# Optimization experiments

Measured on AMD Instinct MI355X. Metric: run time of the kernel, lower is better.

## Reference

```python
import jax, jax.numpy as jnp
import numpy as np

N, E, B = 100000, 1600000, 4
NODE_DIM, EDGE_DIM, H, L, C_DIM = 3, 1, 128, 6, 100


def _mlp2(x, w1, b1, w2, b2):
    # Linear -> ReLU -> Linear
    return jax.nn.relu(x @ w1 + b1) @ w2 + b2


def setup_inputs() -> dict:
    key = jax.random.key(0)
    ks = jax.random.split(key, 32)
    s = 0.02
    inp = {
        "x": jax.random.normal(ks[0], (N, NODE_DIM), jnp.float32),
        "edge_index": jax.random.randint(ks[1], (2, E), 0, N, jnp.int64),
        "edge_attr": jax.random.uniform(ks[2], (E, EDGE_DIM), jnp.float32),
        "t": jax.random.uniform(ks[3], (B,), jnp.float32),
        "batch": jnp.sort(jax.random.randint(ks[4], (N,), 0, B, jnp.int64)),
        "condition": jax.random.normal(ks[5], (B, C_DIM), jnp.float32),
        # input_mlp
        "in_w1": jax.random.normal(ks[6], (NODE_DIM, H), jnp.float32) * s,
        "in_b1": jnp.zeros((H,), jnp.float32),
        "in_w2": jax.random.normal(ks[7], (H, H), jnp.float32) * s,
        "in_b2": jnp.zeros((H,), jnp.float32),
        # time_mlp
        "t_w1": jax.random.normal(ks[8], (1, H), jnp.float32) * s,
        "t_b1": jnp.zeros((H,), jnp.float32),
        "t_w2": jax.random.normal(ks[9], (H, H), jnp.float32) * s,
        "t_b2": jnp.zeros((H,), jnp.float32),
        # condition_mlp
        "c_w1": jax.random.normal(ks[10], (C_DIM, H), jnp.float32) * s,
        "c_b1": jnp.zeros((H,), jnp.float32),
        "c_w2": jax.random.normal(ks[11], (H, H), jnp.float32) * s,
        "c_b2": jnp.zeros((H,), jnp.float32),
        # 6 EdgeConv layers, stacked
        "convW1": jax.random.normal(ks[12], (L, 2 * H + EDGE_DIM, H), jnp.float32) * s,
        "convb1": jnp.zeros((L, H), jnp.float32),
        "convW2": jax.random.normal(ks[13], (L, H, H), jnp.float32) * s,
        "convb2": jnp.zeros((L, H), jnp.float32),
        # output_mlp
        "out_w1": jax.random.normal(ks[14], (H, H), jnp.float32) * s,
        "out_b1": jnp.zeros((H,), jnp.float32),
        "out_w2": jax.random.normal(ks[15], (H, NODE_DIM), jnp.float32) * s,
        "out_b2": jnp.zeros((NODE_DIM,), jnp.float32),
    }
    return inp


def reference(x, edge_index, edge_attr, t, batch, condition,
              in_w1, in_b1, in_w2, in_b2,
              t_w1, t_b1, t_w2, t_b2,
              c_w1, c_b1, c_w2, c_b2,
              convW1, convb1, convW2, convb2,
              out_w1, out_b1, out_w2, out_b2):
    n = x.shape[0]
    b = t.shape[0]
    h = _mlp2(x, in_w1, in_b1, in_w2, in_b2)                       # [N,H]
    time_features = _mlp2(t.reshape(b, 1), t_w1, t_b1, t_w2, t_b2)  # [B,H]
    cond_features = _mlp2(condition, c_w1, c_b1, c_w2, c_b2)        # [B,H]
    h = h + time_features[batch] + cond_features[batch]

    src, dst = edge_index[0], edge_index[1]  # PyG: x_j = x[src], x_i = x[dst]
    # in-degree counts for scatter-mean (zero-degree nodes -> mean = 0)
    cnt = jax.ops.segment_sum(jnp.ones((src.shape[0],), h.dtype), dst, num_segments=n)
    inv_cnt = (1.0 / jnp.maximum(cnt, 1.0))[:, None]               # [N,1]

    for i in range(convW1.shape[0]):
        msg_in = jnp.concatenate([h[dst], h[src], edge_attr], axis=1)  # [E, 2H+1]
        msg = _mlp2(msg_in, convW1[i], convb1[i], convW2[i], convb2[i])  # [E,H]
        agg = jax.ops.segment_sum(msg, dst, num_segments=n) * inv_cnt   # scatter-mean
        h = jax.nn.relu(agg) + h

    return _mlp2(h, out_w1, out_b1, out_w2, out_b2)  # [N, node_dim]
```

## Files before the change

### kernel.cpp

```cpp
#include <hip/hip_runtime.h>
#include <hip/hip_fp16.h>

#define HROW 136

typedef _Float16 h4_t __attribute__((ext_vector_type(4)));
typedef _Float16 h8_t __attribute__((ext_vector_type(8)));
typedef float f32x4_t __attribute__((ext_vector_type(4)));

__global__ void k_tc(const float* __restrict__ t, const float* __restrict__ cond,
                     const float* __restrict__ tw1, const float* __restrict__ tb1,
                     const float* __restrict__ tw2, const float* __restrict__ tb2,
                     const float* __restrict__ cw1, const float* __restrict__ cb1,
                     const float* __restrict__ cw2, const float* __restrict__ cb2,
                     float* __restrict__ tf, float* __restrict__ cf, int B, int CDIM)
{
    __shared__ float hidT[8][128];
    __shared__ float hidC[8][128];
    int j = threadIdx.x;
    for (int b = 0; b < B; ++b) {
        hidT[b][j] = fmaxf(t[b] * tw1[j] + tb1[j], 0.f);
        float s = cb1[j];
        for (int d = 0; d < CDIM; ++d) s += cond[b * CDIM + d] * cw1[d * 128 + j];
        hidC[b][j] = fmaxf(s, 0.f);
    }
    __syncthreads();
    for (int b = 0; b < B; ++b) {
        float s1 = tb2[j], s2 = cb2[j];
        for (int k = 0; k < 128; ++k) {
            s1 += hidT[b][k] * tw2[k * 128 + j];
            s2 += hidC[b][k] * cw2[k * 128 + j];
        }
        tf[b * 128 + j] = s1;
        cf[b * 128 + j] = s2;
    }
}

__global__ void k_prep(const float* __restrict__ convW1, const float* __restrict__ convW2,
                       _Float16* __restrict__ w2t, _Float16* __restrict__ w1at,
                       _Float16* __restrict__ w1bt, int total)
{
    int idx = blockIdx.x * 256 + threadIdx.x;
    if (idx >= total) return;
    int i = idx >> 14;
    int jk = idx & 16383;
    int j = jk >> 7, k = jk & 127;
    w2t[idx]  = (_Float16)convW2[(size_t)i * 16384 + k * 128 + j];
    w1at[idx] = (_Float16)convW1[(size_t)i * 32896 + k * 128 + j];
    w1bt[idx] = (_Float16)convW1[(size_t)i * 32896 + 16384 + k * 128 + j];
}

__global__ void k_prep2(const float* __restrict__ in_w2, const float* __restrict__ out_w1,
                        _Float16* __restrict__ in_w2t, _Float16* __restrict__ ow1t)
{
    int idx = blockIdx.x * 256 + threadIdx.x;
    int which = idx >> 14;
    int jk = idx & 16383;
    int j = jk >> 7, k = jk & 127;
    if (which == 0) in_w2t[jk] = (_Float16)in_w2[k * 128 + j];
    else            ow1t[jk]  = (_Float16)out_w1[k * 128 + j];
}

__global__ void k_count(const int* __restrict__ dst, int* __restrict__ cnt, int E)
{
    int e = blockIdx.x * 256 + threadIdx.x;
    if (e < E) atomicAdd(&cnt[dst[e]], 1);
}

__global__ void k_scan1(const int* __restrict__ cnt, int* __restrict__ bsum, int N)
{
    __shared__ int s[256];
    int i = blockIdx.x * 256 + threadIdx.x;
    int c = (i < N) ? cnt[i] : 0;
    s[threadIdx.x] = (c + 1) & ~1;
    __syncthreads();
    for (int d = 128; d > 0; d >>= 1) {
        if (threadIdx.x < d) s[threadIdx.x] += s[threadIdx.x + d];
        __syncthreads();
    }
    if (threadIdx.x == 0) bsum[blockIdx.x] = s[0];
}

__global__ void k_scan2(const int* __restrict__ bsum, int* __restrict__ boff, int NB)
{
    __shared__ int s[512];
    int t = threadIdx.x;
    int v = (t < NB) ? bsum[t] : 0;
    s[t] = v;
    __syncthreads();
    for (int d = 1; d < 512; d <<= 1) {
        int x = (t >= d) ? s[t - d] : 0;
        __syncthreads();
        s[t] += x;
        __syncthreads();
    }
    if (t < NB) boff[t] = s[t] - v;
}

__global__ void k_scan3(const int* __restrict__ cnt, const int* __restrict__ boff,
                        int* __restrict__ off, int N)
{
    __shared__ int s[256];
    int t = threadIdx.x;
    int i = blockIdx.x * 256 + t;
    int c = (i < N) ? cnt[i] : 0;
    int v = (c + 1) & ~1;
    s[t] = v;
    __syncthreads();
    for (int d = 1; d < 256; d <<= 1) {
        int x = (t >= d) ? s[t - d] : 0;
        __syncthreads();
        s[t] += x;
        __syncthreads();
    }
    if (i < N) off[i] = boff[blockIdx.x] + s[t] - v;
}

__global__ void k_fill(const int* __restrict__ src, const int* __restrict__ dst,
                       const float* __restrict__ ea, const int* __restrict__ off,
                       int* __restrict__ cur, int2* __restrict__ csr, int E)
{
    int e = blockIdx.x * 256 + threadIdx.x;
    if (e < E) {
        int d = dst[e];
        int r = atomicAdd(&cur[d], 1);
        int2 v;
        v.x = src[e];
        v.y = __float_as_int(ea[e]);
        csr[off[d] + r] = v;
    }
}

__device__ __forceinline__ h8_t load_frag(const _Float16* p)
{
    h4_t lo = *(const h4_t*)p;
    h4_t hi = *(const h4_t*)(p + 16);
    h8_t f;
    f[0] = lo[0]; f[1] = lo[1]; f[2] = lo[2]; f[3] = lo[3];
    f[4] = hi[0]; f[5] = hi[1]; f[6] = hi[2]; f[7] = hi[3];
    return f;
}

__device__ __forceinline__ void mfma_gemm64(const _Float16* Al, const _Float16* Wl,
                                            f32x4_t acc[8], int wnt0, int l)
{
    int r16 = l & 15, g4 = (l >> 4) * 4;
    const _Float16* ap = Al + r16 * HROW + g4;
    const _Float16* bp = Wl + (wnt0 * 16 + r16) * HROW + g4;
    #pragma unroll
    for (int ks = 0; ks < 4; ++ks) {
        h8_t b0 = load_frag(bp + ks * 32);
        h8_t b1 = load_frag(bp + 16 * HROW + ks * 32);
        #pragma unroll
        for (int mt = 0; mt < 4; ++mt) {
            h8_t a = load_frag(ap + mt * 16 * HROW + ks * 32);
            acc[mt * 2 + 0] = __builtin_amdgcn_mfma_f32_16x16x32_f16(a, b0, acc[mt * 2 + 0], 0, 0, 0);
            acc[mt * 2 + 1] = __builtin_amdgcn_mfma_f32_16x16x32_f16(a, b1, acc[mt * 2 + 1], 0, 0, 0);
        }
    }
}

__device__ __forceinline__ void stage_w(_Float16* Wl, const _Float16* __restrict__ Wg, int t)
{
    for (int i = t; i < 2048; i += 256) {
        int row = i >> 4, c8 = (i & 15) * 8;
        *(uint4*)&Wl[row * HROW + c8] = *(const uint4*)&Wg[row * 128 + c8];
    }
}

__device__ __forceinline__ void stage_ah(_Float16* Al, const _Float16* __restrict__ g,
                                         int bn0, int N, int t)
{
    for (int i = t; i < 64 * 16; i += 256) {
        int nn = i >> 4, c8 = (i & 15) * 8;
        int n = bn0 + nn;
        uint4 v = {0u, 0u, 0u, 0u};
        if (n < N) v = *(const uint4*)&g[(size_t)n * 128 + c8];
        *(uint4*)&Al[nn * HROW + c8] = v;
    }
}

#define ZERO8(acc) \
    { _Pragma("unroll") for (int z_ = 0; z_ < 8; ++z_) acc[z_] = (f32x4_t){0.f, 0.f, 0.f, 0.f}; }

__global__ __launch_bounds__(256, 3) void k_fused_mfma(
    float* __restrict__ h, const _Float16* S, const int* __restrict__ cnt,
    const _Float16* __restrict__ w2t, const float* __restrict__ b2,
    const _Float16* __restrict__ w1at, const _Float16* __restrict__ w1bt,
    const float* __restrict__ b1n,
    _Float16* P, _Float16* Q, int N)
{
    __shared__ _Float16 Al[64 * HROW];
    __shared__ _Float16 Wl[128 * HROW];
    int bn0 = blockIdx.x * 64;
    int t = threadIdx.x;
    int l = t & 63, wv = t >> 6;
    int wnt0 = wv * 2;
    int r16 = l & 15, g4r = (l >> 4) * 4;

    stage_ah(Al, S, bn0, N, t);
    stage_w(Wl, w2t, t);
    __syncthreads();

    f32x4_t acc[8];
    ZERO8(acc);
    mfma_gemm64(Al, Wl, acc, wnt0, l);

    float hn[8][4];
    #pragma unroll
    for (int q = 0; q < 2; ++q) {
        int j = (wnt0 + q) * 16 + r16;
        float b2v = b2[j];
        #pragma unroll
        for (int mt = 0; mt < 4; ++mt) {
            #pragma unroll
            for (int r = 0; r < 4; ++r) {
                int n = bn0 + mt * 16 + g4r + r;
                float v = 0.f;
                if (n < N) {
                    float agg = acc[mt * 2 + q][r] + b2v;
                    int c = cnt[n];
                    float rr = (c > 0) ? fmaxf(agg, 0.f) : 0.f;
                    v = h[(size_t)n * 128 + j] + rr;
                    h[(size_t)n * 128 + j] = v;
                }
                hn[mt * 2 + q][r] = v;
            }
        }
    }
    __syncthreads();

    #pragma unroll
    for (int q = 0; q < 2; ++q) {
        int j = (wnt0 + q) * 16 + r16;
        #pragma unroll
        for (int mt = 0; mt < 4; ++mt)
            #pragma unroll
            for (int r = 0; r < 4; ++r)
                Al[(mt * 16 + g4r + r) * HROW + j] = (_Float16)hn[mt * 2 + q][r];
    }
    stage_w(Wl, w1at, t);
    __syncthreads();

    ZERO8(acc);
    mfma_gemm64(Al, Wl, acc, wnt0, l);
    #pragma unroll
    for (int q = 0; q < 2; ++q) {
        int j = (wnt0 + q) * 16 + r16;
        float b1v = b1n[j];
        #pragma unroll
        for (int mt = 0; mt < 4; ++mt)
            #pragma unroll
            for (int r = 0; r < 4; ++r) {
                int n = bn0 + mt * 16 + g4r + r;
                if (n < N) P[(size_t)n * 128 + j] = (_Float16)(acc[mt * 2 + q][r] + b1v);
            }
    }
    __syncthreads();

    stage_w(Wl, w1bt, t);
    __syncthreads();

    ZERO8(acc);
    mfma_gemm64(Al, Wl, acc, wnt0, l);
    #pragma unroll
    for (int q = 0; q < 2; ++q) {
        int j = (wnt0 + q) * 16 + r16;
        #pragma unroll
        for (int mt = 0; mt < 4; ++mt)
            #pragma unroll
            for (int r = 0; r < 4; ++r) {
                int n = bn0 + mt * 16 + g4r + r;
                if (n < N) Q[(size_t)n * 128 + j] = (_Float16)acc[mt * 2 + q][r];
            }
    }
}

__global__ __launch_bounds__(256, 3) void k_input_pq_mfma(
    const float* __restrict__ x, const int* __restrict__ batch,
    const float* __restrict__ w1, const float* __restrict__ b1,
    const _Float16* __restrict__ in_w2t, const float* __restrict__ b2,
    const float* __restrict__ tf, const float* __restrict__ cf,
    const _Float16* __restrict__ w1at0, const _Float16* __restrict__ w1bt0,
    const float* __restrict__ b1n,
    float* __restrict__ h, _Float16* __restrict__ P, _Float16* __restrict__ Q, int N)
{
    __shared__ _Float16 Al[64 * HROW];
    __shared__ _Float16 Wl[128 * HROW];
    __shared__ float xs[192];
    __shared__ int   bs[64];
    int bn0 = blockIdx.x * 64;
    int t = threadIdx.x;
    int l = t & 63, wv = t >> 6;
    int wnt0 = wv * 2;
    int r16 = l & 15, g4r = (l >> 4) * 4;

    if (t < 192) {
        int nn = t / 3, d = t - nn * 3;
        int n = bn0 + nn;
        xs[t] = (n < N) ? x[(size_t)n * 3 + d] : 0.f;
    }
    if (t < 64) {
        int n = bn0 + t;
        bs[t] = (n < N) ? batch[n] : 0;
    }
    __syncthreads();
    for (int idx = t; idx < 64 * 128; idx += 256) {
        int nn = idx >> 7, k = idx & 127;
        float hid = fmaxf(xs[nn * 3] * w1[k] + xs[nn * 3 + 1] * w1[128 + k]
                          + xs[nn * 3 + 2] * w1[256 + k] + b1[k], 0.f);
        Al[nn * HROW + k] = (_Float16)hid;
    }
    stage_w(Wl, in_w2t, t);
    __syncthreads();

    f32x4_t acc[8];
    ZERO8(acc);
    mfma_gemm64(Al, Wl, acc, wnt0, l);

    float hn[8][4];
    #pragma unroll
    for (int q = 0; q < 2; ++q) {
        int j = (wnt0 + q) * 16 + r16;
        float b2v = b2[j];
        #pragma unroll
        for (int mt = 0; mt < 4; ++mt) {
            #pragma unroll
            for (int r = 0; r < 4; ++r) {
                int nl = mt * 16 + g4r + r;
                int n = bn0 + nl;
                float v = 0.f;
                if (n < N) {
                    int b = bs[nl];
                    v = acc[mt * 2 + q][r] + b2v + tf[b * 128 + j] + cf[b * 128 + j];
                    h[(size_t)n * 128 + j] = v;
                }
                hn[mt * 2 + q][r] = v;
            }
        }
    }
    __syncthreads();

    #pragma unroll
    for (int q = 0; q < 2; ++q) {
        int j = (wnt0 + q) * 16 + r16;
        #pragma unroll
        for (int mt = 0; mt < 4; ++mt)
            #pragma unroll
            for (int r = 0; r < 4; ++r)
                Al[(mt * 16 + g4r + r) * HROW + j] = (_Float16)hn[mt * 2 + q][r];
    }
    stage_w(Wl, w1at0, t);
    __syncthreads();

    ZERO8(acc);
    mfma_gemm64(Al, Wl, acc, wnt0, l);
    #pragma unroll
    for (int q = 0; q < 2; ++q) {
        int j = (wnt0 + q) * 16 + r16;
        float b1v = b1n[j];
        #pragma unroll
        for (int mt = 0; mt < 4; ++mt)
            #pragma unroll
            for (int r = 0; r < 4; ++r) {
                int n = bn0 + mt * 16 + g4r + r;
                if (n < N) P[(size_t)n * 128 + j] = (_Float16)(acc[mt * 2 + q][r] + b1v);
            }
    }
    __syncthreads();

    stage_w(Wl, w1bt0, t);
    __syncthreads();

    ZERO8(acc);
    mfma_gemm64(Al, Wl, acc, wnt0, l);
    #pragma unroll
    for (int q = 0; q < 2; ++q) {
        int j = (wnt0 + q) * 16 + r16;
        #pragma unroll
        for (int mt = 0; mt < 4; ++mt)
            #pragma unroll
            for (int r = 0; r < 4; ++r) {
                int n = bn0 + mt * 16 + g4r + r;
                if (n < N) Q[(size_t)n * 128 + j] = (_Float16)acc[mt * 2 + q][r];
            }
    }
}

__global__ __launch_bounds__(256, 3) void k_final_mfma(
    const float* __restrict__ h, const _Float16* S, const int* __restrict__ cnt,
    const _Float16* __restrict__ w2t, const float* __restrict__ b2,
    const _Float16* __restrict__ ow1t, const float* __restrict__ ob1,
    const float* __restrict__ ow2, const float* __restrict__ ob2,
    float* __restrict__ out, int N)
{
    __shared__ _Float16 Al[64 * HROW];
    __shared__ _Float16 Wl[128 * HROW];
    int bn0 = blockIdx.x * 64;
    int t = threadIdx.x;
    int l = t & 63, wv = t >> 6;
    int wnt0 = wv * 2;
    int r16 = l & 15, g4r = (l >> 4) * 4;

    stage_ah(Al, S, bn0, N, t);
    stage_w(Wl, w2t, t);
    __syncthreads();

    f32x4_t acc[8];
    ZERO8(acc);
    mfma_gemm64(Al, Wl, acc, wnt0, l);

    float hn[8][4];
    #pragma unroll
    for (int q = 0; q < 2; ++q) {
        int j = (wnt0 + q) * 16 + r16;
        float b2v = b2[j];
        #pragma unroll
        for (int mt = 0; mt < 4; ++mt) {
            #pragma unroll
            for (int r = 0; r < 4; ++r) {
                int n = bn0 + mt * 16 + g4r + r;
                float v = 0.f;
                if (n < N) {
                    float agg = acc[mt * 2 + q][r] + b2v;
                    int c = cnt[n];
                    float rr = (c > 0) ? fmaxf(agg, 0.f) : 0.f;
                    v = h[(size_t)n * 128 + j] + rr;
                }
                hn[mt * 2 + q][r] = v;
            }
        }
    }
    __syncthreads();

    #pragma unroll
    for (int q = 0; q < 2; ++q) {
        int j = (wnt0 + q) * 16 + r16;
        #pragma unroll
        for (int mt = 0; mt < 4; ++mt)
            #pragma unroll
            for (int r = 0; r < 4; ++r)
                Al[(mt * 16 + g4r + r) * HROW + j] = (_Float16)hn[mt * 2 + q][r];
    }
    stage_w(Wl, ow1t, t);
    __syncthreads();

    ZERO8(acc);
    mfma_gemm64(Al, Wl, acc, wnt0, l);
    __syncthreads();

    #pragma unroll
    for (int q = 0; q < 2; ++q) {
        int j = (wnt0 + q) * 16 + r16;
        float b1v = ob1[j];
        #pragma unroll
        for (int mt = 0; mt < 4; ++mt)
            #pragma unroll
            for (int r = 0; r < 4; ++r)
                Al[(mt * 16 + g4r + r) * HROW + j] = (_Float16)fmaxf(acc[mt * 2 + q][r] + b1v, 0.f);
    }
    __syncthreads();

    if (t < 192) {
        int nn = t / 3, d = t - nn * 3;
        int n = bn0 + nn;
        if (n < N) {
            float s = ob2[d];
            for (int j = 0; j < 128; ++j)
                s += (float)Al[nn * HROW + j] * ow2[j * 3 + d];
            out[(size_t)n * 3 + d] = s;
        }
    }
}

__global__ __launch_bounds__(256) void k_edge(
    _Float16* PS, const __half* __restrict__ Q,
    const int2* __restrict__ csr, const int* __restrict__ off, const int* __restrict__ cnt,
    const float* __restrict__ W1, int N)
{
    int n = blockIdx.x * 4 + (threadIdx.x >> 6);
    int lane = threadIdx.x & 63;
    if (n >= N) return;
    int deg = cnt[n];
    int base = off[n];
    const float* w1c = W1 + 256 * 128;
    float2 p = __half22float2(*(const __half2*)&PS[(size_t)n * 128 + lane * 2]);
    float2 w = *(const float2*)&w1c[lane * 2];
    const __half* Ql = Q + lane * 2;
    float accx = 0.f, accy = 0.f;
    int e = 0;
    for (; e + 8 <= deg; e += 8) {
        const int4* c4 = (const int4*)(csr + base + e);
        int4 ca = c4[0], cb = c4[1], cc = c4[2], cd = c4[3];
        float2 q0 = __half22float2(*(const __half2*)&Ql[(size_t)ca.x * 128]);
        float2 q1 = __half22float2(*(const __half2*)&Ql[(size_t)ca.z * 128]);
        float2 q2 = __half22float2(*(const __half2*)&Ql[(size_t)cb.x * 128]);
        float2 q3 = __half22float2(*(const __half2*)&Ql[(size_t)cb.z * 128]);
        float2 q4 = __half22float2(*(const __half2*)&Ql[(size_t)cc.x * 128]);
        float2 q5 = __half22float2(*(const __half2*)&Ql[(size_t)cc.z * 128]);
        float2 q6 = __half22float2(*(const __half2*)&Ql[(size_t)cd.x * 128]);
        float2 q7 = __half22float2(*(const __half2*)&Ql[(size_t)cd.z * 128]);
        float e0 = __int_as_float(ca.y), e1 = __int_as_float(ca.w);
        float e2 = __int_as_float(cb.y), e3 = __int_as_float(cb.w);
        float e4 = __int_as_float(cc.y), e5 = __int_as_float(cc.w);
        float e6 = __int_as_float(cd.y), e7 = __int_as_float(cd.w);
        accx += fmaxf(p.x + q0.x + e0 * w.x, 0.f);
        accy += fmaxf(p.y + q0.y + e0 * w.y, 0.f);
        accx += fmaxf(p.x + q1.x + e1 * w.x, 0.f);
        accy += fmaxf(p.y + q1.y + e1 * w.y, 0.f);
        accx += fmaxf(p.x + q2.x + e2 * w.x, 0.f);
        accy += fmaxf(p.y + q2.y + e2 * w.y, 0.f);
        accx += fmaxf(p.x + q3.x + e3 * w.x, 0.f);
        accy += fmaxf(p.y + q3.y + e3 * w.y, 0.f);
        accx += fmaxf(p.x + q4.x + e4 * w.x, 0.f);
        accy += fmaxf(p.y + q4.y + e4 * w.y, 0.f);
        accx += fmaxf(p.x + q5.x + e5 * w.x, 0.f);
        accy += fmaxf(p.y + q5.y + e5 * w.y, 0.f);
        accx += fmaxf(p.x + q6.x + e6 * w.x, 0.f);
        accy += fmaxf(p.y + q6.y + e6 * w.y, 0.f);
        accx += fmaxf(p.x + q7.x + e7 * w.x, 0.f);
        accy += fmaxf(p.y + q7.y + e7 * w.y, 0.f);
    }
    if (e + 4 <= deg) {
        const int4* c4 = (const int4*)(csr + base + e);
        int4 ca = c4[0], cb = c4[1];
        float2 q0 = __half22float2(*(const __half2*)&Ql[(size_t)ca.x * 128]);
        float2 q1 = __half22float2(*(const __half2*)&Ql[(size_t)ca.z * 128]);
        float2 q2 = __half22float2(*(const __half2*)&Ql[(size_t)cb.x * 128]);
        float2 q3 = __half22float2(*(const __half2*)&Ql[(size_t)cb.z * 128]);
        float e0 = __int_as_float(ca.y), e1 = __int_as_float(ca.w);
        float e2 = __int_as_float(cb.y), e3 = __int_as_float(cb.w);
        accx += fmaxf(p.x + q0.x + e0 * w.x, 0.f);
        accy += fmaxf(p.y + q0.y + e0 * w.y, 0.f);
        accx += fmaxf(p.x + q1.x + e1 * w.x, 0.f);
        accy += fmaxf(p.y + q1.y + e1 * w.y, 0.f);
        accx += fmaxf(p.x + q2.x + e2 * w.x, 0.f);
        accy += fmaxf(p.y + q2.y + e2 * w.y, 0.f);
        accx += fmaxf(p.x + q3.x + e3 * w.x, 0.f);
        accy += fmaxf(p.y + q3.y + e3 * w.y, 0.f);
        e += 4;
    }
    if (e + 2 <= deg) {
        const int4* c4 = (const int4*)(csr + base + e);
        int4 ca = c4[0];
        float2 q0 = __half22float2(*(const __half2*)&Ql[(size_t)ca.x * 128]);
        float2 q1 = __half22float2(*(const __half2*)&Ql[(size_t)ca.z * 128]);
        float e0 = __int_as_float(ca.y), e1 = __int_as_float(ca.w);
        accx += fmaxf(p.x + q0.x + e0 * w.x, 0.f);
        accy += fmaxf(p.y + q0.y + e0 * w.y, 0.f);
        accx += fmaxf(p.x + q1.x + e1 * w.x, 0.f);
        accy += fmaxf(p.y + q1.y + e1 * w.y, 0.f);
        e += 2;
    }
    if (e < deg) {
        int2 c = csr[base + e];
        float2 q = __half22float2(*(const __half2*)&Ql[(size_t)c.x * 128]);
        float ec = __int_as_float(c.y);
        accx += fmaxf(p.x + q.x + ec * w.x, 0.f);
        accy += fmaxf(p.y + q.y + ec * w.y, 0.f);
    }
    float invc = 1.f / (float)max(deg, 1);
    *(__half2*)&PS[(size_t)n * 128 + lane * 2] = __floats2half2_rn(accx * invc, accy * invc);
}

extern "C" void kernel_launch(void* const* d_in, const int* in_sizes, int n_in,
                              void* d_out, int out_size, void* d_ws, size_t ws_size,
                              hipStream_t stream)
{
    const float* x         = (const float*)d_in[0];
    const int*   edge_idx  = (const int*)d_in[1];
    const float* edge_attr = (const float*)d_in[2];
    const float* tt        = (const float*)d_in[3];
    const int*   batch     = (const int*)d_in[4];
    const float* cond      = (const float*)d_in[5];
    const float* in_w1 = (const float*)d_in[6],  *in_b1 = (const float*)d_in[7];
    const float* in_w2 = (const float*)d_in[8],  *in_b2 = (const float*)d_in[9];
    const float* t_w1  = (const float*)d_in[10], *t_b1  = (const float*)d_in[11];
    const float* t_w2  = (const float*)d_in[12], *t_b2  = (const float*)d_in[13];
    const float* c_w1  = (const float*)d_in[14], *c_b1  = (const float*)d_in[15];
    const float* c_w2  = (const float*)d_in[16], *c_b2  = (const float*)d_in[17];
    const float* convW1 = (const float*)d_in[18], *convb1 = (const float*)d_in[19];
    const float* convW2 = (const float*)d_in[20], *convb2 = (const float*)d_in[21];
    const float* out_w1 = (const float*)d_in[22], *out_b1 = (const float*)d_in[23];
    const float* out_w2 = (const float*)d_in[24], *out_b2 = (const float*)d_in[25];

    const int N = in_sizes[0] / 3;
    const int E = in_sizes[1] / 2;
    const int B = in_sizes[3];
    const int CDIM = in_sizes[5] / B;
    const int L = in_sizes[19] / 128;

    const int* esrc = edge_idx;
    const int* edst = edge_idx + E;

    char* w = (char*)d_ws;
    auto alloc = [&](size_t bytes) -> char* {
        char* p = w;
        w += (bytes + 255) & ~(size_t)255;
        return p;
    };
    float*     h      = (float*)alloc((size_t)N * 128 * 4);
    _Float16*  Pp     = (_Float16*)alloc((size_t)N * 128 * 2);
    _Float16*  Q      = (_Float16*)alloc((size_t)N * 128 * 2);
    int*       cnt    = (int*)alloc((size_t)N * 4);
    int*       cur    = (int*)alloc((size_t)N * 4);
    int*       off    = (int*)alloc((size_t)N * 4);
    int*       bsum   = (int*)alloc(4096);
    int*       boff   = (int*)alloc(4096);
    int2*      csr    = (int2*)alloc(((size_t)E + N + 8) * 8);
    float*     tf     = (float*)alloc((size_t)B * 128 * 4);
    float*     cf     = (float*)alloc((size_t)B * 128 * 4);
    _Float16*  w2t    = (_Float16*)alloc((size_t)L * 16384 * 2);
    _Float16*  w1at   = (_Float16*)alloc((size_t)L * 16384 * 2);
    _Float16*  w1bt   = (_Float16*)alloc((size_t)L * 16384 * 2);
    _Float16*  in_w2t = (_Float16*)alloc(16384 * 2);
    _Float16*  ow1t   = (_Float16*)alloc(16384 * 2);

    hipMemsetAsync(cnt, 0, (size_t)N * 4, stream);
    hipMemsetAsync(cur, 0, (size_t)N * 4, stream);

    k_tc<<<1, 128, 0, stream>>>(tt, cond, t_w1, t_b1, t_w2, t_b2,
                                c_w1, c_b1, c_w2, c_b2, tf, cf, B, CDIM);

    const int prepTot = L * 16384;
    k_prep<<<(prepTot + 255) / 256, 256, 0, stream>>>(convW1, convW2, w2t, w1at, w1bt, prepTot);
    k_prep2<<<128, 256, 0, stream>>>(in_w2, out_w1, in_w2t, ow1t);

    const int eb = (E + 255) / 256;
    const int nb = (N + 255) / 256;
    k_count<<<eb, 256, 0, stream>>>(edst, cnt, E);
    k_scan1<<<nb, 256, 0, stream>>>(cnt, bsum, N);
    k_scan2<<<1, 512, 0, stream>>>(bsum, boff, nb);
    k_scan3<<<nb, 256, 0, stream>>>(cnt, boff, off, N);
    k_fill<<<eb, 256, 0, stream>>>(esrc, edst, edge_attr, off, cur, csr, E);

    const int gnodes = (N + 63) / 64;
    k_input_pq_mfma<<<gnodes, 256, 0, stream>>>(x, batch, in_w1, in_b1, in_w2t, in_b2,
                                                tf, cf, w1at, w1bt, convb1, h, Pp, Q, N);

    for (int i = 0; i < L; ++i) {
        const float* b2 = convb2 + (size_t)i * 128;
        k_edge<<<(N + 3) / 4, 256, 0, stream>>>(Pp, (const __half*)Q, csr, off, cnt,
                                                convW1 + (size_t)i * 257 * 128, N);
        if (i < L - 1) {
            const float* b1n = convb1 + (size_t)(i + 1) * 128;
            k_fused_mfma<<<gnodes, 256, 0, stream>>>(h, Pp, cnt,
                                                     w2t + (size_t)i * 16384, b2,
                                                     w1at + (size_t)(i + 1) * 16384,
                                                     w1bt + (size_t)(i + 1) * 16384, b1n,
                                                     Pp, Q, N);
        } else {
            k_final_mfma<<<gnodes, 256, 0, stream>>>(h, Pp, cnt,
                                                     w2t + (size_t)i * 16384, b2,
                                                     ow1t, out_b1, out_w2, out_b2,
                                                     (float*)d_out, N);
        }
    }
}
```

Measured before the change: 1.100 ms.

## Load MFMA B-fragments directly from global in pre-swizzled layout and store h as fp16

Weights are pre-permuted at prep time into the exact per-lane MFMA fragment order, so each wave reads its B fragments straight from global/L2 with one 16-byte load instead of staging a 128x136 weight tile in LDS. This drops the weight LDS buffer and several block barriers, and raises the occupancy hint from 3 to 6 blocks per CU. The residual state h is also stored in fp16 instead of fp32, halving its read/write traffic. The costs are repeated global weight loads per block, which rely on cache hits, and reduced precision in the residual accumulation across layers.

Result: slower. 1.417 ms (+28.8%).

```diff
diff --git a/kernel.cpp b/kernel.cpp
--- a/kernel.cpp
+++ b/kernel.cpp
@@ -35,6 +35,16 @@
     }
 }
 
+__device__ __forceinline__ int frag_off(int j, int k)
+{
+    int nt = j >> 4, ks = k >> 5, kl = k & 31;
+    int hi = (kl >= 16) ? 1 : 0;
+    int k4 = kl - hi * 16;
+    int l = ((k4 >> 2) << 4) | (j & 15);
+    int e = (k4 & 3) + hi * 4;
+    return ((nt * 4 + ks) * 64 + l) * 8 + e;
+}
+
 __global__ void k_prep(const float* __restrict__ convW1, const float* __restrict__ convW2,
                        _Float16* __restrict__ w2t, _Float16* __restrict__ w1at,
                        _Float16* __restrict__ w1bt, int total)
@@ -44,9 +54,11 @@
     int i = idx >> 14;
     int jk = idx & 16383;
     int j = jk >> 7, k = jk & 127;
-    w2t[idx]  = (_Float16)convW2[(size_t)i * 16384 + k * 128 + j];
-    w1at[idx] = (_Float16)convW1[(size_t)i * 32896 + k * 128 + j];
-    w1bt[idx] = (_Float16)convW1[(size_t)i * 32896 + 16384 + k * 128 + j];
+    int off = frag_off(j, k);
+    size_t base = (size_t)i * 16384;
+    w2t[base + off]  = (_Float16)convW2[base + (size_t)k * 128 + j];
+    w1at[base + off] = (_Float16)convW1[(size_t)i * 32896 + (size_t)k * 128 + j];
+    w1bt[base + off] = (_Float16)convW1[(size_t)i * 32896 + 16384 + (size_t)k * 128 + j];
 }
 
 __global__ void k_prep2(const float* __restrict__ in_w2, const float* __restrict__ out_w1,
@@ -56,8 +68,9 @@
     int which = idx >> 14;
     int jk = idx & 16383;
     int j = jk >> 7, k = jk & 127;
-    if (which == 0) in_w2t[jk] = (_Float16)in_w2[k * 128 + j];
-    else            ow1t[jk]  = (_Float16)out_w1[k * 128 + j];
+    int off = frag_off(j, k);
+    if (which == 0) in_w2t[off] = (_Float16)in_w2[k * 128 + j];
+    else            ow1t[off]  = (_Float16)out_w1[k * 128 + j];
 }
 
 __global__ void k_count(const int* __restrict__ dst, int* __restrict__ cnt, int E)
@@ -140,30 +153,22 @@
     return f;
 }
 
-__device__ __forceinline__ void mfma_gemm64(const _Float16* Al, const _Float16* Wl,
-                                            f32x4_t acc[8], int wnt0, int l)
+__device__ __forceinline__ void mfma_gemm64g(const _Float16* Al,
+                                             const _Float16* __restrict__ Wf,
+                                             f32x4_t acc[8], int wnt0, int l)
 {
     int r16 = l & 15, g4 = (l >> 4) * 4;
     const _Float16* ap = Al + r16 * HROW + g4;
-    const _Float16* bp = Wl + (wnt0 * 16 + r16) * HROW + g4;
     #pragma unroll
     for (int ks = 0; ks < 4; ++ks) {
-        h8_t b0 = load_frag(bp + ks * 32);
-        h8_t b1 = load_frag(bp + 16 * HROW + ks * 32);
+        h8_t b0 = *(const h8_t*)&Wf[(((wnt0 + 0) * 4 + ks) * 64 + l) * 8];
+        h8_t b1 = *(const h8_t*)&Wf[(((wnt0 + 1) * 4 + ks) * 64 + l) * 8];
         #pragma unroll
         for (int mt = 0; mt < 4; ++mt) {
             h8_t a = load_frag(ap + mt * 16 * HROW + ks * 32);
             acc[mt * 2 + 0] = __builtin_amdgcn_mfma_f32_16x16x32_f16(a, b0, acc[mt * 2 + 0], 0, 0, 0);
             acc[mt * 2 + 1] = __builtin_amdgcn_mfma_f32_16x16x32_f16(a, b1, acc[mt * 2 + 1], 0, 0, 0);
         }
-    }
-}
-
-__device__ __forceinline__ void stage_w(_Float16* Wl, const _Float16* __restrict__ Wg, int t)
-{
-    for (int i = t; i < 2048; i += 256) {
-        int row = i >> 4, c8 = (i & 15) * 8;
-        *(uint4*)&Wl[row * HROW + c8] = *(const uint4*)&Wg[row * 128 + c8];
     }
 }
 
@@ -182,15 +187,14 @@
 #define ZERO8(acc) \
     { _Pragma("unroll") for (int z_ = 0; z_ < 8; ++z_) acc[z_] = (f32x4_t){0.f, 0.f, 0.f, 0.f}; }
 
-__global__ __launch_bounds__(256, 3) void k_fused_mfma(
-    float* __restrict__ h, const _Float16* S, const int* __restrict__ cnt,
+__global__ __launch_bounds__(256, 6) void k_fused_mfma(
+    _Float16* __restrict__ h, const _Float16* S, const int* __restrict__ cnt,
     const _Float16* __restrict__ w2t, const float* __restrict__ b2,
     const _Float16* __restrict__ w1at, const _Float16* __restrict__ w1bt,
     const float* __restrict__ b1n,
     _Float16* P, _Float16* Q, int N)
 {
     __shared__ _Float16 Al[64 * HROW];
-    __shared__ _Float16 Wl[128 * HROW];
     int bn0 = blockIdx.x * 64;
     int t = threadIdx.x;
     int l = t & 63, wv = t >> 6;
@@ -198,12 +202,11 @@
     int r16 = l & 15, g4r = (l >> 4) * 4;
 
     stage_ah(Al, S, bn0, N, t);
-    stage_w(Wl, w2t, t);
     __syncthreads();
 
     f32x4_t acc[8];
     ZERO8(acc);
-    mfma_gemm64(Al, Wl, acc, wnt0, l);
+    mfma_gemm64g(Al, w2t, acc, wnt0, l);
 
     float hn[8][4];
     #pragma unroll
@@ -220,8 +223,8 @@
                     float agg = acc[mt * 2 + q][r] + b2v;
                     int c = cnt[n];
                     float rr = (c > 0) ? fmaxf(agg, 0.f) : 0.f;
-                    v = h[(size_t)n * 128 + j] + rr;
-                    h[(size_t)n * 128 + j] = v;
+                    v = (float)h[(size_t)n * 128 + j] + rr;
+                    h[(size_t)n * 128 + j] = (_Float16)v;
                 }
                 hn[mt * 2 + q][r] = v;
             }
@@ -238,11 +241,10 @@
             for (int r = 0; r < 4; ++r)
                 Al[(mt * 16 + g4r + r) * HROW + j] = (_Float16)hn[mt * 2 + q][r];
     }
-    stage_w(Wl, w1at, t);
-    __syncthreads();
-
-    ZERO8(acc);
-    mfma_gemm64(Al, Wl, acc, wnt0, l);
+    __syncthreads();
+
+    ZERO8(acc);
+    mfma_gemm64g(Al, w1at, acc, wnt0, l);
     #pragma unroll
     for (int q = 0; q < 2; ++q) {
         int j = (wnt0 + q) * 16 + r16;
@@ -255,13 +257,9 @@
                 if (n < N) P[(size_t)n * 128 + j] = (_Float16)(acc[mt * 2 + q][r] + b1v);
             }
     }
-    __syncthreads();
-
-    stage_w(Wl, w1bt, t);
-    __syncthreads();
-
-    ZERO8(acc);
-    mfma_gemm64(Al, Wl, acc, wnt0, l);
+
+    ZERO8(acc);
+    mfma_gemm64g(Al, w1bt, acc, wnt0, l);
     #pragma unroll
     for (int q = 0; q < 2; ++q) {
         int j = (wnt0 + q) * 16 + r16;
@@ -275,17 +273,16 @@
     }
 }
 
-__global__ __launch_bounds__(256, 3) void k_input_pq_mfma(
+__global__ __launch_bounds__(256, 6) void k_input_pq_mfma(
     const float* __restrict__ x, const int* __restrict__ batch,
     const float* __restrict__ w1, const float* __restrict__ b1,
     const _Float16* __restrict__ in_w2t, const float* __restrict__ b2,
     const float* __restrict__ tf, const float* __restrict__ cf,
     const _Float16* __restrict__ w1at0, const _Float16* __restrict__ w1bt0,
     const float* __restrict__ b1n,
-    float* __restrict__ h, _Float16* __restrict__ P, _Float16* __restrict__ Q, int N)
+    _Float16* __restrict__ h, _Float16* __restrict__ P, _Float16* __restrict__ Q, int N)
 {
     __shared__ _Float16 Al[64 * HROW];
-    __shared__ _Float16 Wl[128 * HROW];
     __shared__ float xs[192];
     __shared__ int   bs[64];
     int bn0 = blockIdx.x * 64;
@@ -310,12 +307,11 @@
                           + xs[nn * 3 + 2] * w1[256 + k] + b1[k], 0.f);
         Al[nn * HROW + k] = (_Float16)hid;
     }
-    stage_w(Wl, in_w2t, t);
     __syncthreads();
 
     f32x4_t acc[8];
     ZERO8(acc);
-    mfma_gemm64(Al, Wl, acc, wnt0, l);
+    mfma_gemm64g(Al, in_w2t, acc, wnt0, l);
 
     float hn[8][4];
     #pragma unroll
@@ -332,7 +328,7 @@
                 if (n < N) {
                     int b = bs[nl];
                     v = acc[mt * 2 + q][r] + b2v + tf[b * 128 + j] + cf[b * 128 + j];
-                    h[(size_t)n * 128 + j] = v;
+                    h[(size_t)n * 128 + j] = (_Float16)v;
                 }
                 hn[mt * 2 + q][r] = v;
             }
@@ -349,11 +345,10 @@
             for (int r = 0; r < 4; ++r)
                 Al[(mt * 16 + g4r + r) * HROW + j] = (_Float16)hn[mt * 2 + q][r];
     }
-    stage_w(Wl, w1at0, t);
-    __syncthreads();
-
-    ZERO8(acc);
-    mfma_gemm64(Al, Wl, acc, wnt0, l);
+    __syncthreads();
+
+    ZERO8(acc);
+    mfma_gemm64g(Al, w1at0, acc, wnt0, l);
     #pragma unroll
     for (int q = 0; q < 2; ++q) {
         int j = (wnt0 + q) * 16 + r16;
@@ -366,13 +361,9 @@
                 if (n < N) P[(size_t)n * 128 + j] = (_Float16)(acc[mt * 2 + q][r] + b1v);
             }
     }
-    __syncthreads();
-
-    stage_w(Wl, w1bt0, t);
-    __syncthreads();
-
-    ZERO8(acc);
-    mfma_gemm64(Al, Wl, acc, wnt0, l);
+
+    ZERO8(acc);
+    mfma_gemm64g(Al, w1bt0, acc, wnt0, l);
     #pragma unroll
     for (int q = 0; q < 2; ++q) {
         int j = (wnt0 + q) * 16 + r16;
@@ -386,15 +377,14 @@
     }
 }
 
-__global__ __launch_bounds__(256, 3) void k_final_mfma(
-    const float* __restrict__ h, const _Float16* S, const int* __restrict__ cnt,
+__global__ __launch_bounds__(256, 6) void k_final_mfma(
+    const _Float16* __restrict__ h, const _Float16* S, const int* __restrict__ cnt,
     const _Float16* __restrict__ w2t, const float* __restrict__ b2,
     const _Float16* __restrict__ ow1t, const float* __restrict__ ob1,
     const float* __restrict__ ow2, const float* __restrict__ ob2,
     float* __restrict__ out, int N)
 {
     __shared__ _Float16 Al[64 * HROW];
-    __shared__ _Float16 Wl[128 * HROW];
     int bn0 = blockIdx.x * 64;
     int t = threadIdx.x;
     int l = t & 63, wv = t >> 6;
@@ -402,12 +392,11 @@
     int r16 = l & 15, g4r = (l >> 4) * 4;
 
     stage_ah(Al, S, bn0, N, t);
-    stage_w(Wl, w2t, t);
     __syncthreads();
 
     f32x4_t acc[8];
     ZERO8(acc);
-    mfma_gemm64(Al, Wl, acc, wnt0, l);
+    mfma_gemm64g(Al, w2t, acc, wnt0, l);
 
     float hn[8][4];
     #pragma unroll
@@ -424,7 +413,7 @@
                     float agg = acc[mt * 2 + q][r] + b2v;
                     int c = cnt[n];
                     float rr = (c > 0) ? fmaxf(agg, 0.f) : 0.f;
-                    v = h[(size_t)n * 128 + j] + rr;
+                    v = (float)h[(size_t)n * 128 + j] + rr;
                 }
                 hn[mt * 2 + q][r] = v;
             }
@@ -441,11 +430,10 @@
             for (int r = 0; r < 4; ++r)
                 Al[(mt * 16 + g4r + r) * HROW + j] = (_Float16)hn[mt * 2 + q][r];
     }
-    stage_w(Wl, ow1t, t);
-    __syncthreads();
-
-    ZERO8(acc);
-    mfma_gemm64(Al, Wl, acc, wnt0, l);
+    __syncthreads();
+
+    ZERO8(acc);
+    mfma_gemm64g(Al, ow1t, acc, wnt0, l);
     __syncthreads();
 
     #pragma unroll
@@ -598,7 +586,7 @@
         w += (bytes + 255) & ~(size_t)255;
         return p;
     };
-    float*     h      = (float*)alloc((size_t)N * 128 * 4);
+    _Float16*  h      = (_Float16*)alloc((size_t)N * 128 * 2);
     _Float16*  Pp     = (_Float16*)alloc((size_t)N * 128 * 2);
     _Float16*  Q      = (_Float16*)alloc((size_t)N * 128 * 2);
     int*       cnt    = (int*)alloc((size_t)N * 4);
```
